# Kernel tuning notes

Measured on AMD Instinct MI355X. Metric: run time of the kernel, lower is better.

The kernel has to match this reference:

```python
import jax, jax.numpy as jnp
import numpy as np

B, N, NIN, NHID, D = 8, 2048, 256, 256, 64  # head = 1 (required by squeeze())


def setup_inputs() -> dict:
    key = jax.random.key(0)
    ks = jax.random.split(key, 12)
    xn = lambda k, shape, s=1.0: jax.random.normal(k, shape, jnp.float32) * s
    xav = lambda fi, fo: (2.0 / (fi + fo)) ** 0.5  # xavier_normal std
    return {
        "inputs": xn(ks[0], (B, N, NIN)),
        "fc1_w": xn(ks[1], (NHID, NIN), xav(NIN, NHID)),
        "fc1_b": jnp.full((NHID,), 0.1, jnp.float32),
        "fc2_w": xn(ks[2], (NHID, NHID), xav(NHID, NHID)),
        "fc2_b": jnp.full((NHID,), 0.1, jnp.float32),
        "bn_g": 1.0 + 0.1 * xn(ks[3], (NHID,)),
        "bn_b": 0.1 * xn(ks[4], (NHID,)),
        "bn_mean": 0.1 * xn(ks[5], (NHID,)),
        "bn_var": jax.random.uniform(ks[6], (NHID,), jnp.float32, 0.5, 1.5),
        "wq_w": xn(ks[7], (D, NHID), xav(NHID, D)),
        "wq_b": jnp.full((D,), 0.1, jnp.float32),
        "wk_w": xn(ks[8], (D, NHID), xav(NHID, D)),
        "wk_b": jnp.full((D,), 0.1, jnp.float32),
        "mlp2_w": xn(ks[9], (1, 2 * D), xav(2 * D, 1)),
        "mlp2_b": jnp.full((1,), 0.1, jnp.float32),
    }


def reference(inputs, fc1_w, fc1_b, fc2_w, fc2_b, bn_g, bn_b, bn_mean, bn_var,
              wq_w, wq_b, wk_w, wk_b, mlp2_w, mlp2_b):
    # MLP: Linear -> ELU -> (dropout off, eval) -> Linear -> ELU -> BatchNorm1d (eval, running stats)
    x = jax.nn.elu(jnp.einsum('bni,hi->bnh', inputs, fc1_w) + fc1_b)
    x = jax.nn.elu(jnp.einsum('bnh,oh->bno', x, fc2_w) + fc2_b)
    X = (x - bn_mean) * jax.lax.rsqrt(bn_var + 1e-5) * bn_g + bn_b  # [B,N,NHID]
    # Q/K projections (head=1 -> shapes [B,N,D])
    Xq = jnp.einsum('bnh,dh->bnd', X, wq_w) + wq_b
    Xk = jnp.einsum('bnh,dh->bnd', X, wk_w) + wk_b
    # Original: cat([NK, NQ], -1) over all (i,j) pairs then Linear(2D -> 1).
    # Algebraically identical decomposition: probs[b,i,j] = Xk[b,j].wk_half + Xq[b,i].wq_half + bias
    wk_half, wq_half = mlp2_w[0, :D], mlp2_w[0, D:]
    sk = Xk @ wk_half  # [B,N]  (varies with j, the K/column index)
    sq = Xq @ wq_half  # [B,N]  (varies with i, the Q/row index)
    probs = sq[:, :, None] + sk[:, None, :] + mlp2_b[0]  # [B,N,N]
    return probs
```

## Files before the change

kernel.cpp:

```cpp
#include <hip/hip_runtime.h>
#include <hip/hip_bf16.h>
#include <math.h>

typedef __bf16 bf16x8 __attribute__((ext_vector_type(8)));
typedef float  f32x4  __attribute__((ext_vector_type(4)));
typedef unsigned int u32;
typedef u32 u32x4 __attribute__((ext_vector_type(4)));
typedef unsigned short u16;

#define WS_UQ    0
#define WS_UK    256
#define WS_CONST 512
#define WS_SQ    528
#define WS_SK    16912

__device__ __forceinline__ float elu1(float x) {
    return x > 0.f ? x : (__expf(x) - 1.f);
}

__global__ void prep_all(const float* __restrict__ w1, const float* __restrict__ w2,
                         const float* __restrict__ bn_g, const float* __restrict__ bn_b,
                         const float* __restrict__ bn_mean, const float* __restrict__ bn_var,
                         const float* __restrict__ wq_w, const float* __restrict__ wq_b,
                         const float* __restrict__ wk_w, const float* __restrict__ wk_b,
                         const float* __restrict__ mlp2_w, const float* __restrict__ mlp2_b,
                         float* __restrict__ ws, float* __restrict__ outb) {
    if (blockIdx.x == 0) {
        __shared__ float redq[256], redk[256];
        const int h = threadIdx.x;
        float s  = bn_g[h] * rsqrtf(bn_var[h] + 1e-5f);
        float tt = bn_b[h] - bn_mean[h] * s;
        float vq = 0.f, vk = 0.f;
        #pragma unroll
        for (int d = 0; d < 64; ++d) {
            vq += wq_w[d * 256 + h] * mlp2_w[64 + d];
            vk += wk_w[d * 256 + h] * mlp2_w[d];
        }
        ws[WS_UQ + h] = s * vq;
        ws[WS_UK + h] = s * vk;
        redq[h] = tt * vq;
        redk[h] = tt * vk;
        __syncthreads();
        for (int st = 128; st > 0; st >>= 1) {
            if (h < st) { redq[h] += redq[h + st]; redk[h] += redk[h + st]; }
            __syncthreads();
        }
        if (h == 0) {
            float cq = 0.f, ck = 0.f;
            for (int d = 0; d < 64; ++d) {
                cq += wq_b[d] * mlp2_w[64 + d];
                ck += wk_b[d] * mlp2_w[d];
            }
            ws[WS_CONST + 0] = redq[0] + cq;
            ws[WS_CONST + 1] = redk[0] + ck;
            ws[WS_CONST + 2] = mlp2_b[0];
        }
        return;
    }
    const int bid = blockIdx.x - 1;
    const int m   = bid >> 3;
    const int kt  = bid & 7;
    const float* src = m ? w2 : w1;
    __bf16* stg = (__bf16*)outb + m * 65536;
    const int tid = threadIdx.x;
    #pragma unroll
    for (int it = 0; it < 4; ++it) {
        int idx = it * 256 + tid;
        int nt = idx >> 6, l = idx & 63;
        int lr = l & 15, lk = l >> 4;
        const float* sp = src + (nt * 16 + lr) * 256 + kt * 32 + lk * 8;
        bf16x8 hi;
        #pragma unroll
        for (int j = 0; j < 8; ++j) hi[j] = (__bf16)sp[j];
        *(bf16x8*)(stg + (kt * 16 + nt) * 512 + l * 8) = hi;
    }
}

__global__ __launch_bounds__(256) void main_mfma(const float* __restrict__ inp,
                                                 const float* __restrict__ b1,
                                                 const float* __restrict__ b2,
                                                 float* __restrict__ ws,
                                                 const float* __restrict__ outb) {
    __shared__ u32 X1p[4096];
    __shared__ float redq[64], redk[64];

    const int tid = threadIdx.x;
    const int l   = tid & 63;
    const int w   = tid >> 6;
    const int lr  = l & 15;
    const int lk  = l >> 4;
    const int rows0 = blockIdx.x * 16;
    const int n0  = w * 64;

    const __bf16* s1 = (const __bf16*)outb;
    const __bf16* s2 = s1 + 65536;
    const float*  arow = inp + (size_t)(rows0 + lr) * 256 + lk * 8;

    f32x4 acc[4];

    #pragma unroll
    for (int nt = 0; nt < 4; ++nt) acc[nt] = (f32x4)0.f;

    bf16x8 bc[4];
    float4 f0, f1;
    #pragma unroll
    for (int nt = 0; nt < 4; ++nt)
        bc[nt] = *(const bf16x8*)(s1 + ((0 * 16 + w * 4 + nt) << 9) + l * 8);
    f0 = ((const float4*)arow)[0];
    f1 = ((const float4*)arow)[1];

    #pragma unroll
    for (int kt = 0; kt < 8; ++kt) {
        bf16x8 bn[4];
        float4 g0 = f0, g1 = f1;
        if (kt < 7) {
            #pragma unroll
            for (int nt = 0; nt < 4; ++nt)
                bn[nt] = *(const bf16x8*)(s1 + (((kt + 1) * 16 + w * 4 + nt) << 9) + l * 8);
            g0 = ((const float4*)(arow + (kt + 1) * 32))[0];
            g1 = ((const float4*)(arow + (kt + 1) * 32))[1];
        } else {
            #pragma unroll
            for (int nt = 0; nt < 4; ++nt) bn[nt] = bc[nt];
        }
        bf16x8 ah, al;
        {
            float fv[8] = {f0.x,f0.y,f0.z,f0.w,f1.x,f1.y,f1.z,f1.w};
            #pragma unroll
            for (int j = 0; j < 8; ++j) {
                __bf16 hv = (__bf16)fv[j];
                ah[j] = hv;
                al[j] = (__bf16)(fv[j] - (float)hv);
            }
        }
        #pragma unroll
        for (int nt = 0; nt < 4; ++nt) {
            acc[nt] = __builtin_amdgcn_mfma_f32_16x16x32_bf16(ah, bc[nt], acc[nt], 0, 0, 0);
            acc[nt] = __builtin_amdgcn_mfma_f32_16x16x32_bf16(al, bc[nt], acc[nt], 0, 0, 0);
        }
        #pragma unroll
        for (int nt = 0; nt < 4; ++nt) bc[nt] = bn[nt];
        f0 = g0; f1 = g1;
    }
    #pragma unroll
    for (int nt = 0; nt < 4; ++nt) {
        int col = n0 + nt * 16 + lr;
        float bb = b1[col];
        #pragma unroll
        for (int r = 0; r < 4; ++r) {
            int row = lk * 4 + r;
            float v = elu1(acc[nt][r] + bb);
            __bf16 hv = (__bf16)v;
            __bf16 lv = (__bf16)(v - (float)hv);
            u32 pk = ((u32)__builtin_bit_cast(u16, hv) << 16) | __builtin_bit_cast(u16, lv);
            int ob = row * 1024 + ((col * 4) ^ (row << 4));
            *(u32*)((char*)X1p + ob) = pk;
        }
    }
    __syncthreads();

    #pragma unroll
    for (int nt = 0; nt < 4; ++nt) acc[nt] = (f32x4)0.f;

    const int base = lr * 1024;
    const int sw   = lr << 4;

    bf16x8 bc2[4];
    #pragma unroll
    for (int nt = 0; nt < 4; ++nt)
        bc2[nt] = *(const bf16x8*)(s2 + ((0 * 16 + w * 4 + nt) << 9) + l * 8);

    #pragma unroll
    for (int kt = 0; kt < 8; ++kt) {
        bf16x8 bn[4];
        if (kt < 7) {
            #pragma unroll
            for (int nt = 0; nt < 4; ++nt)
                bn[nt] = *(const bf16x8*)(s2 + (((kt + 1) * 16 + w * 4 + nt) << 9) + l * 8);
        } else {
            #pragma unroll
            for (int nt = 0; nt < 4; ++nt) bn[nt] = bc2[nt];
        }
        int cb = kt * 128 + lk * 32;
        u32x4 q0 = *(const u32x4*)((const char*)X1p + base + (cb ^ sw));
        u32x4 q1 = *(const u32x4*)((const char*)X1p + base + ((cb + 16) ^ sw));
        u32 hw0 = __builtin_amdgcn_perm(q0.y, q0.x, 0x07060302u);
        u32 hw1 = __builtin_amdgcn_perm(q0.w, q0.z, 0x07060302u);
        u32 hw2 = __builtin_amdgcn_perm(q1.y, q1.x, 0x07060302u);
        u32 hw3 = __builtin_amdgcn_perm(q1.w, q1.z, 0x07060302u);
        u32 lw0 = __builtin_amdgcn_perm(q0.y, q0.x, 0x05040100u);
        u32 lw1 = __builtin_amdgcn_perm(q0.w, q0.z, 0x05040100u);
        u32 lw2 = __builtin_amdgcn_perm(q1.y, q1.x, 0x05040100u);
        u32 lw3 = __builtin_amdgcn_perm(q1.w, q1.z, 0x05040100u);
        u32x4 hh = {hw0, hw1, hw2, hw3};
        u32x4 ll = {lw0, lw1, lw2, lw3};
        bf16x8 ah = __builtin_bit_cast(bf16x8, hh);
        bf16x8 al = __builtin_bit_cast(bf16x8, ll);
        #pragma unroll
        for (int nt = 0; nt < 4; ++nt) {
            acc[nt] = __builtin_amdgcn_mfma_f32_16x16x32_bf16(ah, bc2[nt], acc[nt], 0, 0, 0);
            acc[nt] = __builtin_amdgcn_mfma_f32_16x16x32_bf16(al, bc2[nt], acc[nt], 0, 0, 0);
        }
        #pragma unroll
        for (int nt = 0; nt < 4; ++nt) bc2[nt] = bn[nt];
    }

    float sqp[4] = {0.f,0.f,0.f,0.f};
    float skp[4] = {0.f,0.f,0.f,0.f};
    const float* uq = ws + WS_UQ;
    const float* uk = ws + WS_UK;
    #pragma unroll
    for (int nt = 0; nt < 4; ++nt) {
        int col = n0 + nt * 16 + lr;
        float bb = b2[col], qc = uq[col], kc = uk[col];
        #pragma unroll
        for (int r = 0; r < 4; ++r) {
            float v = elu1(acc[nt][r] + bb);
            sqp[r] += v * qc;
            skp[r] += v * kc;
        }
    }
    #pragma unroll
    for (int mm = 8; mm >= 1; mm >>= 1) {
        #pragma unroll
        for (int r = 0; r < 4; ++r) {
            sqp[r] += __shfl_xor(sqp[r], mm);
            skp[r] += __shfl_xor(skp[r], mm);
        }
    }
    if (lr == 0) {
        #pragma unroll
        for (int r = 0; r < 4; ++r) {
            int row = lk * 4 + r;
            redq[w * 16 + row] = sqp[r];
            redk[w * 16 + row] = skp[r];
        }
    }
    __syncthreads();
    if (tid < 16) {
        float s = ws[WS_CONST + 0];
        #pragma unroll
        for (int ww = 0; ww < 4; ++ww) s += redq[ww * 16 + tid];
        ws[WS_SQ + rows0 + tid] = s;
    } else if (tid < 32) {
        int rl = tid - 16;
        float s = ws[WS_CONST + 1];
        #pragma unroll
        for (int ww = 0; ww < 4; ++ww) s += redk[ww * 16 + rl];
        ws[WS_SK + rows0 + rl] = s;
    }
}

__global__ __launch_bounds__(256) void broadcast_out(const float* __restrict__ ws,
                                                     float* __restrict__ out) {
    __shared__ float skL[2048];
    const int bi = blockIdx.x;
    const int b = bi >> 8;
    const int chunk = bi & 255;
    const int tid = threadIdx.x;

    float4* skL4 = (float4*)skL;
    const float4* skb4 = (const float4*)(ws + WS_SK + b * 2048);
    #pragma unroll
    for (int it = 0; it < 2; ++it) skL4[it * 256 + tid] = skb4[it * 256 + tid];
    __syncthreads();

    const float mb = ws[WS_CONST + 2];
    const int i0 = chunk * 8;
    #pragma unroll
    for (int i = 0; i < 8; ++i) {
        float sval = ws[WS_SQ + b * 2048 + i0 + i] + mb;
        float4* orow = (float4*)(out + ((size_t)(b * 2048 + i0 + i)) * 2048);
        #pragma unroll
        for (int hh = 0; hh < 2; ++hh) {
            int j4 = hh * 256 + tid;
            float4 v = skL4[j4];
            orow[j4] = make_float4(sval + v.x, sval + v.y, sval + v.z, sval + v.w);
        }
    }
}

extern "C" void kernel_launch(void* const* d_in, const int* in_sizes, int n_in,
                              void* d_out, int out_size, void* d_ws, size_t ws_size,
                              hipStream_t stream) {
    const float* inputs  = (const float*)d_in[0];
    const float* fc1_w   = (const float*)d_in[1];
    const float* fc1_b   = (const float*)d_in[2];
    const float* fc2_w   = (const float*)d_in[3];
    const float* fc2_b   = (const float*)d_in[4];
    const float* bn_g    = (const float*)d_in[5];
    const float* bn_b    = (const float*)d_in[6];
    const float* bn_mean = (const float*)d_in[7];
    const float* bn_var  = (const float*)d_in[8];
    const float* wq_w    = (const float*)d_in[9];
    const float* wq_b    = (const float*)d_in[10];
    const float* wk_w    = (const float*)d_in[11];
    const float* wk_b    = (const float*)d_in[12];
    const float* mlp2_w  = (const float*)d_in[13];
    const float* mlp2_b  = (const float*)d_in[14];
    float* ws  = (float*)d_ws;
    float* out = (float*)d_out;

    hipLaunchKernelGGL(prep_all, dim3(17), dim3(256), 0, stream,
                       fc1_w, fc2_w, bn_g, bn_b, bn_mean, bn_var,
                       wq_w, wq_b, wk_w, wk_b, mlp2_w, mlp2_b, ws, out);
    hipLaunchKernelGGL(main_mfma, dim3(1024), dim3(256), 0, stream,
                       inputs, fc1_b, fc2_b, ws, out);
    hipLaunchKernelGGL(broadcast_out, dim3(2048), dim3(256), 0, stream, ws, out);
}
```

Measured before the change: 50.67 us.

## Pre-split inputs into packed bf16 hi/lo in prep kernel; simplify broadcast store

The prep kernel gains 256 extra blocks that convert the fp32 input activations into packed hi/lo bf16 pairs. These are stored in the output buffer past the weight staging area. The main MFMA kernel then loads these packed words and extracts the hi and lo halves with byte-permute instructions instead of doing the fp32-to-bf16 split in its inner loop. The broadcast kernel now keeps the sk row in registers instead of shared memory, writes 4 rows per block with nontemporal stores, and launches twice as many blocks. The input pre-pass adds a full extra read and write of the 16 MB input, which may cost more than the conversion ALU work it removes.

```diff
diff --git a/kernel.cpp b/kernel.cpp
--- a/kernel.cpp
+++ b/kernel.cpp
@@ -14,11 +14,20 @@
 #define WS_SQ    528
 #define WS_SK    16912
 
+#define APACK_OFF 262144
+
 __device__ __forceinline__ float elu1(float x) {
     return x > 0.f ? x : (__expf(x) - 1.f);
 }
 
-__global__ void prep_all(const float* __restrict__ w1, const float* __restrict__ w2,
+__device__ __forceinline__ u32 packsplit(float x) {
+    __bf16 h = (__bf16)x;
+    __bf16 l = (__bf16)(x - (float)h);
+    return ((u32)__builtin_bit_cast(u16, h) << 16) | __builtin_bit_cast(u16, l);
+}
+
+__global__ void prep_all(const float* __restrict__ inp,
+                         const float* __restrict__ w1, const float* __restrict__ w2,
                          const float* __restrict__ bn_g, const float* __restrict__ bn_b,
                          const float* __restrict__ bn_mean, const float* __restrict__ bn_var,
                          const float* __restrict__ wq_w, const float* __restrict__ wq_b,
@@ -57,27 +66,39 @@
         }
         return;
     }
-    const int bid = blockIdx.x - 1;
-    const int m   = bid >> 3;
-    const int kt  = bid & 7;
-    const float* src = m ? w2 : w1;
-    __bf16* stg = (__bf16*)outb + m * 65536;
-    const int tid = threadIdx.x;
-    #pragma unroll
-    for (int it = 0; it < 4; ++it) {
-        int idx = it * 256 + tid;
-        int nt = idx >> 6, l = idx & 63;
-        int lr = l & 15, lk = l >> 4;
-        const float* sp = src + (nt * 16 + lr) * 256 + kt * 32 + lk * 8;
-        bf16x8 hi;
-        #pragma unroll
-        for (int j = 0; j < 8; ++j) hi[j] = (__bf16)sp[j];
-        *(bf16x8*)(stg + (kt * 16 + nt) * 512 + l * 8) = hi;
-    }
-}
-
-__global__ __launch_bounds__(256) void main_mfma(const float* __restrict__ inp,
-                                                 const float* __restrict__ b1,
+    if (blockIdx.x <= 16) {
+        const int bid = blockIdx.x - 1;
+        const int m   = bid >> 3;
+        const int kt  = bid & 7;
+        const float* src = m ? w2 : w1;
+        __bf16* stg = (__bf16*)outb + m * 65536;
+        const int tid = threadIdx.x;
+        #pragma unroll
+        for (int it = 0; it < 4; ++it) {
+            int idx = it * 256 + tid;
+            int nt = idx >> 6, l = idx & 63;
+            int lr = l & 15, lk = l >> 4;
+            const float* sp = src + (nt * 16 + lr) * 256 + kt * 32 + lk * 8;
+            bf16x8 hi;
+            #pragma unroll
+            for (int j = 0; j < 8; ++j) hi[j] = (__bf16)sp[j];
+            *(bf16x8*)(stg + (kt * 16 + nt) * 512 + l * 8) = hi;
+        }
+        return;
+    }
+    const int gtid = (blockIdx.x - 17) * 256 + threadIdx.x;
+    const float4* in4 = (const float4*)inp;
+    u32x4* ap4 = (u32x4*)((u32*)outb + APACK_OFF);
+    #pragma unroll
+    for (int it = 0; it < 16; ++it) {
+        int idx = it * 65536 + gtid;
+        float4 v = in4[idx];
+        u32x4 o = {packsplit(v.x), packsplit(v.y), packsplit(v.z), packsplit(v.w)};
+        ap4[idx] = o;
+    }
+}
+
+__global__ __launch_bounds__(256) void main_mfma(const float* __restrict__ b1,
                                                  const float* __restrict__ b2,
                                                  float* __restrict__ ws,
                                                  const float* __restrict__ outb) {
@@ -94,7 +115,8 @@
 
     const __bf16* s1 = (const __bf16*)outb;
     const __bf16* s2 = s1 + 65536;
-    const float*  arow = inp + (size_t)(rows0 + lr) * 256 + lk * 8;
+    const u32x4* arow4 = (const u32x4*)((const u32*)outb + APACK_OFF) +
+                         ((size_t)(rows0 + lr) * 64 + lk * 2);
 
     f32x4 acc[4];
 
@@ -102,37 +124,39 @@
     for (int nt = 0; nt < 4; ++nt) acc[nt] = (f32x4)0.f;
 
     bf16x8 bc[4];
-    float4 f0, f1;
+    u32x4 qa, qb;
     #pragma unroll
     for (int nt = 0; nt < 4; ++nt)
         bc[nt] = *(const bf16x8*)(s1 + ((0 * 16 + w * 4 + nt) << 9) + l * 8);
-    f0 = ((const float4*)arow)[0];
-    f1 = ((const float4*)arow)[1];
+    qa = arow4[0];
+    qb = arow4[1];
 
     #pragma unroll
     for (int kt = 0; kt < 8; ++kt) {
         bf16x8 bn[4];
-        float4 g0 = f0, g1 = f1;
+        u32x4 qan = qa, qbn = qb;
         if (kt < 7) {
             #pragma unroll
             for (int nt = 0; nt < 4; ++nt)
                 bn[nt] = *(const bf16x8*)(s1 + (((kt + 1) * 16 + w * 4 + nt) << 9) + l * 8);
-            g0 = ((const float4*)(arow + (kt + 1) * 32))[0];
-            g1 = ((const float4*)(arow + (kt + 1) * 32))[1];
+            qan = arow4[(kt + 1) * 8];
+            qbn = arow4[(kt + 1) * 8 + 1];
         } else {
             #pragma unroll
             for (int nt = 0; nt < 4; ++nt) bn[nt] = bc[nt];
         }
-        bf16x8 ah, al;
-        {
-            float fv[8] = {f0.x,f0.y,f0.z,f0.w,f1.x,f1.y,f1.z,f1.w};
-            #pragma unroll
-            for (int j = 0; j < 8; ++j) {
-                __bf16 hv = (__bf16)fv[j];
-                ah[j] = hv;
-                al[j] = (__bf16)(fv[j] - (float)hv);
-            }
-        }
+        u32 hw0 = __builtin_amdgcn_perm(qa.y, qa.x, 0x07060302u);
+        u32 hw1 = __builtin_amdgcn_perm(qa.w, qa.z, 0x07060302u);
+        u32 hw2 = __builtin_amdgcn_perm(qb.y, qb.x, 0x07060302u);
+        u32 hw3 = __builtin_amdgcn_perm(qb.w, qb.z, 0x07060302u);
+        u32 lw0 = __builtin_amdgcn_perm(qa.y, qa.x, 0x05040100u);
+        u32 lw1 = __builtin_amdgcn_perm(qa.w, qa.z, 0x05040100u);
+        u32 lw2 = __builtin_amdgcn_perm(qb.y, qb.x, 0x05040100u);
+        u32 lw3 = __builtin_amdgcn_perm(qb.w, qb.z, 0x05040100u);
+        u32x4 hh = {hw0, hw1, hw2, hw3};
+        u32x4 ll = {lw0, lw1, lw2, lw3};
+        bf16x8 ah = __builtin_bit_cast(bf16x8, hh);
+        bf16x8 al = __builtin_bit_cast(bf16x8, ll);
         #pragma unroll
         for (int nt = 0; nt < 4; ++nt) {
             acc[nt] = __builtin_amdgcn_mfma_f32_16x16x32_bf16(ah, bc[nt], acc[nt], 0, 0, 0);
@@ -140,7 +164,7 @@
         }
         #pragma unroll
         for (int nt = 0; nt < 4; ++nt) bc[nt] = bn[nt];
-        f0 = g0; f1 = g1;
+        qa = qan; qb = qbn;
     }
     #pragma unroll
     for (int nt = 0; nt < 4; ++nt) {
@@ -150,9 +174,7 @@
         for (int r = 0; r < 4; ++r) {
             int row = lk * 4 + r;
             float v = elu1(acc[nt][r] + bb);
-            __bf16 hv = (__bf16)v;
-            __bf16 lv = (__bf16)(v - (float)hv);
-            u32 pk = ((u32)__builtin_bit_cast(u16, hv) << 16) | __builtin_bit_cast(u16, lv);
+            u32 pk = packsplit(v);
             int ob = row * 1024 + ((col * 4) ^ (row << 4));
             *(u32*)((char*)X1p + ob) = pk;
         }
@@ -253,30 +275,25 @@
 
 __global__ __launch_bounds__(256) void broadcast_out(const float* __restrict__ ws,
                                                      float* __restrict__ out) {
-    __shared__ float skL[2048];
-    const int bi = blockIdx.x;
-    const int b = bi >> 8;
-    const int chunk = bi & 255;
+    const int bi  = blockIdx.x;
+    const int b   = bi >> 9;
+    const int i0  = (bi & 511) * 4;
     const int tid = threadIdx.x;
 
-    float4* skL4 = (float4*)skL;
-    const float4* skb4 = (const float4*)(ws + WS_SK + b * 2048);
-    #pragma unroll
-    for (int it = 0; it < 2; ++it) skL4[it * 256 + tid] = skb4[it * 256 + tid];
-    __syncthreads();
-
+    const f32x4* skb4 = (const f32x4*)(ws + WS_SK + b * 2048);
+    f32x4 v0 = skb4[tid];
+    f32x4 v1 = skb4[tid + 256];
     const float mb = ws[WS_CONST + 2];
-    const int i0 = chunk * 8;
-    #pragma unroll
-    for (int i = 0; i < 8; ++i) {
-        float sval = ws[WS_SQ + b * 2048 + i0 + i] + mb;
-        float4* orow = (float4*)(out + ((size_t)(b * 2048 + i0 + i)) * 2048);
-        #pragma unroll
-        for (int hh = 0; hh < 2; ++hh) {
-            int j4 = hh * 256 + tid;
-            float4 v = skL4[j4];
-            orow[j4] = make_float4(sval + v.x, sval + v.y, sval + v.z, sval + v.w);
-        }
+    const float* sqb = ws + WS_SQ + b * 2048 + i0;
+
+    #pragma unroll
+    for (int i = 0; i < 4; ++i) {
+        float sval = sqb[i] + mb;
+        f32x4* orow = (f32x4*)(out + ((size_t)(b * 2048 + i0 + i)) * 2048);
+        f32x4 o0 = {sval + v0.x, sval + v0.y, sval + v0.z, sval + v0.w};
+        f32x4 o1 = {sval + v1.x, sval + v1.y, sval + v1.z, sval + v1.w};
+        __builtin_nontemporal_store(o0, &orow[tid]);
+        __builtin_nontemporal_store(o1, &orow[tid + 256]);
     }
 }
 
@@ -301,10 +318,10 @@
     float* ws  = (float*)d_ws;
     float* out = (float*)d_out;
 
-    hipLaunchKernelGGL(prep_all, dim3(17), dim3(256), 0, stream,
-                       fc1_w, fc2_w, bn_g, bn_b, bn_mean, bn_var,
+    hipLaunchKernelGGL(prep_all, dim3(273), dim3(256), 0, stream,
+                       inputs, fc1_w, fc2_w, bn_g, bn_b, bn_mean, bn_var,
                        wq_w, wq_b, wk_w, wk_b, mlp2_w, mlp2_b, ws, out);
     hipLaunchKernelGGL(main_mfma, dim3(1024), dim3(256), 0, stream,
-                       inputs, fc1_b, fc2_b, ws, out);
-    hipLaunchKernelGGL(broadcast_out, dim3(2048), dim3(256), 0, stream, ws, out);
-}
+                       fc1_b, fc2_b, ws, out);
+    hipLaunchKernelGGL(broadcast_out, dim3(4096), dim3(256), 0, stream, ws, out);
+}
```

Measured after the change: 59.19 us. 1.17x slower.
